# Optimization experiments

Hardware: AMD Instinct MI355X
Metric: run time of the kernel (lower is better)

Reference implementation:

```python
import jax, jax.numpy as jnp
import numpy as np

NEG = -1e30  # log-space 'zero' (avoid real -inf for stable exp/grad)


def _ctc_loss_mean(logp, targets, target_lengths, blank):
    """CTC loss, PyTorch semantics (reduction='mean', zero_infinity=True).
    logp: (B, T, V) log-probabilities; targets: (B, L) padded labels;
    target_lengths: (B,) ints. All input lengths are T (uniform here).
    """
    B, T, V = logp.shape
    L = targets.shape[1]
    S = 2 * L + 1  # extended label length: blank-interleaved

    ext = jnp.full((B, S), blank, dtype=targets.dtype)
    ext = ext.at[:, 1::2].set(targets)  # blanks at even s, labels at odd s

    s = jnp.arange(S)
    valid = s[None, :] < (2 * target_lengths + 1)[:, None]  # (B, S)
    prev2 = jnp.pad(ext[:, :-2], ((0, 0), (2, 0)), constant_values=blank)
    # skip transition s-2 -> s allowed only at non-blank s with no label repeat
    allow_skip = (s[None, :] >= 2) & (ext != blank) & (ext != prev2)

    # per-(t, s) emission log-prob, masked outside valid extended labels
    emit = jnp.take_along_axis(
        logp, jnp.broadcast_to(ext[:, None, :], (B, T, S)), axis=2
    )  # (B, T, S)
    emit = jnp.where(valid[:, None, :], emit, NEG)

    alpha0 = jnp.full((B, S), NEG, dtype=logp.dtype)
    alpha0 = alpha0.at[:, 0].set(emit[:, 0, 0])
    alpha0 = alpha0.at[:, 1].set(emit[:, 0, 1])

    def step(alpha, e):
        a1 = alpha
        a2 = jnp.pad(alpha[:, :-1], ((0, 0), (1, 0)), constant_values=NEG)
        a3 = jnp.pad(alpha[:, :-2], ((0, 0), (2, 0)), constant_values=NEG)
        a3 = jnp.where(allow_skip, a3, NEG)
        m = jnp.maximum(jnp.maximum(a1, a2), a3)
        new = m + jnp.log(jnp.exp(a1 - m) + jnp.exp(a2 - m) + jnp.exp(a3 - m)) + e
        return new, None

    alpha, _ = jax.lax.scan(step, alpha0, jnp.swapaxes(emit, 0, 1)[1:])

    i1 = (2 * target_lengths).astype(jnp.int32)
    l1 = jnp.take_along_axis(alpha, i1[:, None], axis=1)[:, 0]
    l2 = jnp.take_along_axis(alpha, jnp.maximum(i1 - 1, 0)[:, None], axis=1)[:, 0]
    l2 = jnp.where(target_lengths > 0, l2, NEG)
    m = jnp.maximum(l1, l2)
    loss = -(m + jnp.log(jnp.exp(l1 - m) + jnp.exp(l2 - m)))  # (B,)
    loss = jnp.where(loss > 1e20, 0.0, loss)  # zero_infinity=True
    # reduction='mean': divide by target length, then batch mean
    return jnp.mean(loss / jnp.maximum(target_lengths, 1).astype(loss.dtype))


def setup_inputs() -> dict:
    key = jax.random.key(0)
    kl, kt, kn = jax.random.split(key, 3)
    B, T, V, L = 32, 1024, 1000, 256
    logits = jax.random.normal(kl, (B, T, V), dtype=jnp.float32)
    targets = jax.random.randint(kt, (B, L), 1, V).astype(jnp.int32)
    lengths = jax.random.randint(kn, (B,), L // 2 + 2, L + 1)
    target_padding_mask = jnp.arange(L)[None, :] < lengths[:, None]  # bool (B, L)
    return {"logits": logits, "targets": targets,
            "target_padding_mask": target_padding_mask}


def reference(logits, targets, target_padding_mask):
    blank = 0
    lg = logits[:, :-1, :]            # drop last frame
    tgt = targets[:, 1:]              # drop leading (SOS) token
    logp = jax.nn.log_softmax(lg, axis=-1)  # (B, T-1, V)
    tlen = target_padding_mask.sum(axis=1).astype(jnp.int32) - 1
    return _ctc_loss_mean(logp, tgt, tlen, blank)
```

## Files before the change

kernel.cpp:

```cpp
#include <hip/hip_runtime.h>

#define LOG2E 1.4426950408889634f
#define LN2   0.6931471805599453

static constexpr int B  = 32;
static constexpr int T  = 1024;
static constexpr int TT = 1023;
static constexpr int V  = 1000;
static constexpr int L  = 256;
static constexpr int S  = 511;
static constexpr int SP = 512;
static constexpr int TP = 1024;

using h8  = __attribute__((ext_vector_type(8))) _Float16;
using f4  = __attribute__((ext_vector_type(4))) float;
using i4  = __attribute__((ext_vector_type(4))) int;

__device__ __forceinline__ float fexp2(float x) {
#if __has_builtin(__builtin_amdgcn_exp2f)
  return __builtin_amdgcn_exp2f(x);
#else
  return exp2f(x);
#endif
}
__device__ __forceinline__ float flog2(float x) {
#if __has_builtin(__builtin_amdgcn_logf)
  return __builtin_amdgcn_logf(x);
#else
  return log2f(x);
#endif
}

#if __has_builtin(__builtin_amdgcn_update_dpp)
__device__ __forceinline__ float shr1f(float x) {
  int r = __builtin_amdgcn_update_dpp(0, __float_as_int(x), 0x138, 0xf, 0xf, true);
  return __int_as_float(r);
}
__device__ __forceinline__ int shl1i(int x) {
  return __builtin_amdgcn_update_dpp(0, x, 0x130, 0xf, 0xf, true);
}
#define DPP_SWITCH(T, OLD, SRC, BC)                                            \
  T r;                                                                         \
  switch (ctrl) {                                                              \
    case 0x111: r = __builtin_amdgcn_update_dpp(OLD, SRC, 0x111, 0xf, 0xf, BC); break; \
    case 0x112: r = __builtin_amdgcn_update_dpp(OLD, SRC, 0x112, 0xf, 0xf, BC); break; \
    case 0x114: r = __builtin_amdgcn_update_dpp(OLD, SRC, 0x114, 0xf, 0xf, BC); break; \
    case 0x118: r = __builtin_amdgcn_update_dpp(OLD, SRC, 0x118, 0xf, 0xf, BC); break; \
    case 0x142: r = __builtin_amdgcn_update_dpp(OLD, SRC, 0x142, 0xf, 0xf, BC); break; \
    default:    r = __builtin_amdgcn_update_dpp(OLD, SRC, 0x143, 0xf, 0xf, BC); break; \
  }

__device__ __forceinline__ int dppmax_step(int m, const int ctrl) {
  DPP_SWITCH(int, 0, m, true);
  return max(m, r);
}
__device__ __forceinline__ int wavemax_to_sgpr(int m) {
  m = dppmax_step(m, 0x111);
  m = dppmax_step(m, 0x112);
  m = dppmax_step(m, 0x114);
  m = dppmax_step(m, 0x118);
  m = dppmax_step(m, 0x142);
  m = dppmax_step(m, 0x143);
  return __builtin_amdgcn_readlane(m, 63);
}
__device__ __forceinline__ float dppfmax_step(float x, const int ctrl) {
  int xi = __float_as_int(x);
  DPP_SWITCH(int, xi, xi, false);
  return fmaxf(x, __int_as_float(r));
}
__device__ __forceinline__ float wavefmax(float x) {
  x = dppfmax_step(x, 0x111);
  x = dppfmax_step(x, 0x112);
  x = dppfmax_step(x, 0x114);
  x = dppfmax_step(x, 0x118);
  x = dppfmax_step(x, 0x142);
  x = dppfmax_step(x, 0x143);
  return __int_as_float(__builtin_amdgcn_readlane(__float_as_int(x), 63));
}
__device__ __forceinline__ float dppfadd_step(float x, const int ctrl) {
  DPP_SWITCH(int, 0, __float_as_int(x), true);
  return x + __int_as_float(r);
}
__device__ __forceinline__ float wavefsum(float x) {
  x = dppfadd_step(x, 0x111);
  x = dppfadd_step(x, 0x112);
  x = dppfadd_step(x, 0x114);
  x = dppfadd_step(x, 0x118);
  x = dppfadd_step(x, 0x142);
  x = dppfadd_step(x, 0x143);
  return __int_as_float(__builtin_amdgcn_readlane(__float_as_int(x), 63));
}
#else
__device__ __forceinline__ float shr1f(float x) {
  float r = __shfl_up(x, 1, 64);
  return (threadIdx.x & 63) == 0 ? 0.0f : r;
}
__device__ __forceinline__ int shl1i(int x) {
  int r = __shfl_down(x, 1, 64);
  return (threadIdx.x & 63) == 63 ? 0 : r;
}
__device__ __forceinline__ int wavemax_to_sgpr(int m) {
  for (int o = 32; o >= 1; o >>= 1) m = max(m, __shfl_xor(m, o, 64));
  return m;
}
__device__ __forceinline__ float wavefmax(float x) {
  for (int o = 32; o >= 1; o >>= 1) x = fmaxf(x, __shfl_xor(x, o, 64));
  return x;
}
__device__ __forceinline__ float wavefsum(float x) {
  for (int o = 32; o >= 1; o >>= 1) x += __shfl_xor(x, o, 64);
  return x;
}
#endif

__global__ void k_tlen(const unsigned char* __restrict__ maskb,
                       int* __restrict__ tlen) {
  int b = blockIdx.x;
  int lane = threadIdx.x;
  int ca = 0;
  for (int k = lane; k < L; k += 64) ca += (maskb[b * L + k] != 0) ? 1 : 0;
  for (int o = 32; o >= 1; o >>= 1) ca += __shfl_xor(ca, o, 64);
  int cnt = ca;
  if (ca < 130) {
    const int* mi = (const int*)maskb;
    int cb = 0;
    for (int k = lane; k < L; k += 64) cb += (mi[b * L + k] != 0) ? 1 : 0;
    for (int o = 32; o >= 1; o >>= 1) cb += __shfl_xor(cb, o, 64);
    cnt = cb;
  }
  if (lane == 0) tlen[b] = cnt - 1;
}

__global__ __launch_bounds__(256, 4) void k_emit(const float* __restrict__ logits,
                                                 const int* __restrict__ targets,
                                                 const int* __restrict__ tlenp,
                                                 _Float16* __restrict__ E,
                                                 float* __restrict__ G) {
  __shared__ float yrow[4][1024];
  const int wid = threadIdx.x >> 6;
  const int lane = threadIdx.x & 63;
  float* yw = yrow[wid];
  const int w0 = blockIdx.x * 4 + wid;
  const int sb = lane << 3;

#define EISSUE(P, r)                                              \
  do {                                                            \
    int b_ = (r) / TT;                                            \
    int t_ = (r) - b_ * TT;                                       \
    const float* rp_ = logits + ((size_t)b_ * T + t_) * V + (lane << 2); \
    const int* tp_ = targets + b_ * L + (lane << 2);              \
    const int* lp_ = tlenp + b_;                                  \
    asm volatile(                                                 \
      "global_load_dwordx4 %0, %6, off\n\t"                       \
      "global_load_dwordx4 %1, %6, off offset:1024\n\t"           \
      "global_load_dwordx4 %2, %6, off offset:2048\n\t"           \
      "global_load_dwordx4 %3, %6, off offset:3072\n\t"           \
      "global_load_dwordx4 %4, %7, off\n\t"                       \
      "global_load_dword %5, %8, off"                             \
      : "=&v"(P##u0), "=&v"(P##u1), "=&v"(P##u2), "=&v"(P##u3),   \
        "=&v"(P##tv), "=&v"(P##tl)                                \
      : "v"(rp_), "v"(tp_), "v"(lp_));                            \
  } while (0)

#define EWAIT(n, P)                                               \
  do {                                                            \
    asm volatile("s_waitcnt vmcnt(" #n ")"                        \
                 : "+v"(P##u0), "+v"(P##u1), "+v"(P##u2),         \
                   "+v"(P##u3), "+v"(P##tv), "+v"(P##tl));        \
    __builtin_amdgcn_sched_barrier(0);                            \
  } while (0)

#define EPROC(P, r)                                               \
  do {                                                            \
    int b_ = (r) / TT;                                            \
    int t_ = (r) - b_ * TT;                                       \
    f4 v0 = P##u0 * LOG2E;                                        \
    f4 v1 = P##u1 * LOG2E;                                        \
    f4 v2 = P##u2 * LOG2E;                                        \
    f4 v3 = P##u3 * LOG2E;                                        \
    const bool has3 = (lane < 58);         \
    if (!has3) { v3[0] = v3[1] = v3[2] = v3[3] = -2.0e30f; }      \
    reinterpret_cast<f4*>(yw)[lane]       = v0;                   \
    reinterpret_cast<f4*>(yw)[lane + 64]  = v1;                   \
    reinterpret_cast<f4*>(yw)[lane + 128] = v2;                   \
    if (has3) reinterpret_cast<f4*>(yw)[lane + 192] = v3;         \
    float lm = fmaxf(fmaxf(fmaxf(v0[0], v0[1]), fmaxf(v0[2], v0[3])), \
                     fmaxf(fmaxf(v1[0], v1[1]), fmaxf(v1[2], v1[3]))); \
    lm = fmaxf(lm, fmaxf(fmaxf(v2[0], v2[1]), fmaxf(v2[2], v2[3]))); \
    lm = fmaxf(lm, fmaxf(fmaxf(v3[0], v3[1]), fmaxf(v3[2], v3[3]))); \
    const float my = wavefmax(lm);                                \
    float ps = fexp2(v0[0]-my) + fexp2(v0[1]-my) + fexp2(v0[2]-my) + fexp2(v0[3]-my) \
             + fexp2(v1[0]-my) + fexp2(v1[1]-my) + fexp2(v1[2]-my) + fexp2(v1[3]-my) \
             + fexp2(v2[0]-my) + fexp2(v2[1]-my) + fexp2(v2[2]-my) + fexp2(v2[3]-my) \
             + fexp2(v3[0]-my) + fexp2(v3[1]-my) + fexp2(v3[2]-my) + fexp2(v3[3]-my); \
    const float g = -flog2(wavefsum(ps));                         \
    const int smax = 2 * P##tl + 1;                               \
    const int l1 = P##tv[1], l2 = P##tv[2], l3 = P##tv[3];        \
    const int l4 = shl1i(P##tv[0]);              \
    const float eb = fexp2(yw[0]  - my);                          \
    const float e1 = fexp2(yw[l1] - my);                          \
    const float e2 = fexp2(yw[l2] - my);                          \
    const float e3 = fexp2(yw[l3] - my);                          \
    const float e4 = fexp2(yw[l4] - my);                          \
    h8 o;                                                         \
    o[0] = (_Float16)((sb     < smax) ? eb : 0.0f);               \
    o[1] = (_Float16)((sb + 1 < smax) ? e1 : 0.0f);               \
    o[2] = (_Float16)((sb + 2 < smax) ? eb : 0.0f);               \
    o[3] = (_Float16)((sb + 3 < smax) ? e2 : 0.0f);               \
    o[4] = (_Float16)((sb + 4 < smax) ? eb : 0.0f);               \
    o[5] = (_Float16)((sb + 5 < smax) ? e3 : 0.0f);               \
    o[6] = (_Float16)((sb + 6 < smax) ? eb : 0.0f);               \
    o[7] = (_Float16)((lane < 63 && sb + 7 < smax) ? e4 : 0.0f);  \
    reinterpret_cast<h8*>(E + ((size_t)b_ * TP + t_) * SP)[lane] = o; \
    if (lane == 0) G[r] = g;                                      \
  } while (0)

  f4 Au0, Au1, Au2, Au3; i4 Atv; int Atl;
  f4 Bu0, Bu1, Bu2, Bu3; i4 Btv; int Btl;
  f4 Cu0, Cu1, Cu2, Cu3; i4 Ctv; int Ctl;

  EISSUE(A, w0);
  EISSUE(B, w0 + 8184);
  EISSUE(C, w0 + 16368);
  EWAIT(12, A); EPROC(A, w0);
  EISSUE(A, w0 + 24552);
  EWAIT(12, B); EPROC(B, w0 + 8184);
  EWAIT(6,  C); EPROC(C, w0 + 16368);
  EWAIT(0,  A); EPROC(A, w0 + 24552);
#undef EISSUE
#undef EWAIT
#undef EPROC
}

__global__ __launch_bounds__(64, 1) void k_ctc(const _Float16* __restrict__ E,
                                               const int* __restrict__ targets,
                                               const int* __restrict__ tlenp,
                                               const float* __restrict__ G,
                                               float* __restrict__ lossb) {
  const int b = blockIdx.x;
  const int lane = threadIdx.x;
  const int s0 = lane << 3;
  const int* tg = targets + b * L;

  const int tl = tlenp[b];

  double gs = 0.0;
  for (int k = lane; k < TT; k += 64) gs += (double)G[b * TT + k];
  for (int o = 32; o >= 1; o >>= 1) gs += __shfl_xor(gs, o, 64);

  float f1 = 0.0f, f3, f5, f7 = 0.0f;
  {
    int s = s0 + 1;
    if (s >= 3) f1 = (tg[(s + 1) >> 1] != tg[(s - 1) >> 1]) ? 1.0f : 0.0f;
    s = s0 + 3;
    f3 = (tg[(s + 1) >> 1] != tg[(s - 1) >> 1]) ? 1.0f : 0.0f;
    s = s0 + 5;
    f5 = (tg[(s + 1) >> 1] != tg[(s - 1) >> 1]) ? 1.0f : 0.0f;
    s = s0 + 7;
    if (s < S) f7 = (tg[(s + 1) >> 1] != tg[(s - 1) >> 1]) ? 1.0f : 0.0f;
  }

  const _Float16* E0 = E + (size_t)b * TP * SP;
  const _Float16* Ebase = E0 + s0;

  float a0 = (lane == 0) ? (float)E0[0] : 0.0f;
  float a1 = (lane == 0) ? (float)E0[1] : 0.0f;
  float a2 = 0.f, a3 = 0.f, a4 = 0.f, a5 = 0.f, a6 = 0.f, a7 = 0.f;
  float n7 = 0.0f;
  int lsacc = 0;

  asm volatile("" :: "v"(f1), "v"(f3), "v"(f5), "v"(f7),
                     "v"(a0), "v"(a1), "v"(gs), "v"((float)tl));

#define GLROW4(d0, d1, d2, d3, p)                                \
  asm volatile("global_load_dwordx4 %0, %4, off\n\t"             \
               "global_load_dwordx4 %1, %4, off offset:1024\n\t" \
               "global_load_dwordx4 %2, %4, off offset:2048\n\t" \
               "global_load_dwordx4 %3, %4, off offset:3072"     \
               : "=&v"(d0), "=&v"(d1), "=&v"(d2), "=&v"(d3) : "v"(p))

#define LOAD8(P, r0)                                             \
  do {                                                           \
    const _Float16* q_ = Ebase + (size_t)(r0) * SP;              \
    GLROW4(P##0, P##1, P##2, P##3, q_);                          \
    GLROW4(P##4, P##5, P##6, P##7, q_ + 4 * SP);                 \
  } while (0)

#define VMWAIT8(n, P)                                            \
  do {                                                           \
    asm volatile("s_waitcnt vmcnt(" #n ")"                       \
                 : "+v"(P##0), "+v"(P##1), "+v"(P##2), "+v"(P##3), \
                   "+v"(P##4), "+v"(P##5), "+v"(P##6), "+v"(P##7)); \
    __builtin_amdgcn_sched_barrier(0);                           \
  } while (0)

#define STEPF(H)                                                \
  do {                                                          \
    float e7 = (float)(H)[7];                                   \
    float t7 = fmaf(f7, a5, a6 + a7) * e7;                      \
    float n7n = shr1f(t7);                                      \
    float e0 = (float)(H)[0], e1 = (float)(H)[1];               \
    float e2 = (float)(H)[2], e3 = (float)(H)[3];               \
    float e4 = (float)(H)[4], e5 = (float)(H)[5];               \
    float e6 = (float)(H)[6];                                   \
    float t0 = (a0 + n7) * e0;                                  \
    float t1 = fmaf(f1, n7, a0 + a1) * e1;                      \
    float t2 = (a1 + a2) * e2;                                  \
    float t3 = fmaf(f3, a1, a2 + a3) * e3;                      \
    float t4 = (a3 + a4) * e4;                                  \
    float t5 = fmaf(f5, a3, a4 + a5) * e5;                      \
    float t6 = (a5 + a6) * e6;                                  \
    a0 = t0; a1 = t1; a2 = t2; a3 = t3;                         \
    a4 = t4; a5 = t5; a6 = t6; a7 = t7;                         \
    n7 = n7n;                                                   \
  } while (0)

#define RESCALE()                                               \
  do {                                                          \
    int m = max(max(max(__float_as_int(a0), __float_as_int(a1)),\
                    max(__float_as_int(a2), __float_as_int(a3))),\
                max(max(__float_as_int(a4), __float_as_int(a5)),\
                    max(__float_as_int(a6), __float_as_int(a7))));\
    int mw = wavemax_to_sgpr(m);                                \
    int e = mw >> 23;                                           \
    int sh = 229 - e;                                           \
    lsacc += e - 229;                                           \
    a0 = ldexpf(a0, sh); a1 = ldexpf(a1, sh);                   \
    a2 = ldexpf(a2, sh); a3 = ldexpf(a3, sh);                   \
    a4 = ldexpf(a4, sh); a5 = ldexpf(a5, sh);                   \
    a6 = ldexpf(a6, sh); a7 = ldexpf(a7, sh);                   \
    n7 = ldexpf(n7, sh);                                        \
  } while (0)

#define PROC8R(P)                                               \
  do {                                                          \
    RESCALE();                                                  \
    STEPF(P##0); STEPF(P##1); STEPF(P##2); STEPF(P##3);         \
    STEPF(P##4); STEPF(P##5); STEPF(P##6); STEPF(P##7);         \
  } while (0)

  h8 A0, A1, A2, A3, A4, A5, A6, A7;
  h8 B0, B1, B2, B3, B4, B5, B6, B7;
  h8 C0, C1, C2, C3, C4, C5, C6, C7;
  h8 D0, D1, D2, D3, D4, D5, D6, D7;

  LOAD8(A, 1);
  LOAD8(B, 9);
  LOAD8(C, 17);
  LOAD8(D, 25);

  int t = 1;
#pragma unroll 1
  for (int it = 0; it < 30; ++it) {
    VMWAIT8(24, A); PROC8R(A); LOAD8(A, t + 32);
    VMWAIT8(24, B); PROC8R(B); LOAD8(B, t + 40);
    VMWAIT8(24, C); PROC8R(C); LOAD8(C, t + 48);
    VMWAIT8(24, D); PROC8R(D); LOAD8(D, t + 56);
    t += 32;
  }
  VMWAIT8(24, A); PROC8R(A); LOAD8(A, 993);
  VMWAIT8(24, B); PROC8R(B); LOAD8(B, 1001);
  VMWAIT8(24, C); PROC8R(C); LOAD8(C, 1009);
  VMWAIT8(24, D); PROC8R(D); LOAD8(D, 1017);
  VMWAIT8(24, A); PROC8R(A);
  VMWAIT8(16, B); PROC8R(B);
  VMWAIT8(8,  C); PROC8R(C);
  VMWAIT8(0,  D);
  RESCALE();
  STEPF(D0); STEPF(D1); STEPF(D2);
  STEPF(D3); STEPF(D4); STEPF(D5);
#undef GLROW4
#undef LOAD8
#undef VMWAIT8
#undef STEPF
#undef RESCALE
#undef PROC8R

  __shared__ float sal[SP];
  sal[s0 + 0] = a0; sal[s0 + 1] = a1; sal[s0 + 2] = a2; sal[s0 + 3] = a3;
  sal[s0 + 4] = a4; sal[s0 + 5] = a5; sal[s0 + 6] = a6; sal[s0 + 7] = a7;
  __syncthreads();
  if (lane == 0) {
    int i1 = 2 * tl;
    float p = sal[i1] + sal[(i1 > 0 ? i1 : 1) - 1];
    int hi = __float_as_int(p);
    int ep = (hi >> 23) - 127;
    float pm = ldexpf(p, -ep);
    float lm = flog2(pm);
    double loss2 = -((double)lm + (double)ep + (double)lsacc + gs);
    float loss = (float)(loss2 * LN2);
    if (!(loss <= 1e20f)) loss = 0.0f;
    int dv = (tl > 0) ? tl : 1;
    lossb[b] = loss / (float)dv;
  }
}

__global__ void k_mean(const float* __restrict__ lossb, float* __restrict__ out) {
  int lane = threadIdx.x;
  float v = (lane < B) ? lossb[lane] : 0.0f;
  for (int o = 32; o >= 1; o >>= 1) v += __shfl_xor(v, o, 64);
  if (lane == 0) out[0] = v / (float)B;
}

extern "C" void kernel_launch(void* const* d_in, const int* in_sizes, int n_in,
                              void* d_out, int out_size, void* d_ws, size_t ws_size,
                              hipStream_t stream) {
  const float* logits = (const float*)d_in[0];
  const int* targets = (const int*)d_in[1];
  const unsigned char* mask = (const unsigned char*)d_in[2];

  char* ws = (char*)d_ws;
  int* tlen = (int*)ws;
  float* lossb = (float*)(ws + 128);
  float* G = (float*)(ws + 512);
  _Float16* E = (_Float16*)(ws + 512 + 132 * 1024);

  k_tlen<<<B, 64, 0, stream>>>(mask, tlen);
  k_emit<<<(B * TT) / 16, 256, 0, stream>>>(logits, targets, tlen, E, G);
  k_ctc<<<B, 64, 0, stream>>>(E, targets, tlen, G, lossb);
  k_mean<<<1, 64, 0, stream>>>(lossb, (float*)d_out);
}
```

Before: 99.98 us.

## Fuse f16 emission convert into multiply via fma_mix and rescale less often

Replaces the separate f16-to-f32 convert plus multiply in each recurrence step with a single v_fma_mix_f32 that reads the packed half directly. It also moves the wave-wide max rescale from every 8 steps to every 32 steps, lowering the target exponent so the values have headroom to avoid overflow over the longer interval. The final loss gather now uses register shuffles instead of an LDS write, barrier and read. Rescaling less often risks underflow or overflow in the scaled probability domain.

```diff
diff --git a/kernel.cpp b/kernel.cpp
--- a/kernel.cpp
+++ b/kernel.cpp
@@ -294,22 +294,34 @@
     __builtin_amdgcn_sched_barrier(0);                           \
   } while (0)
 
+#define MIXLO(D, SSS, HWORD)                                     \
+  asm("v_fma_mix_f32 %0, %1, %2, 0 op_sel:[0,0,0] op_sel_hi:[0,1,0]" \
+      : "=v"(D) : "v"(SSS), "v"(HWORD))
+#define MIXHI(D, SSS, HWORD)                                     \
+  asm("v_fma_mix_f32 %0, %1, %2, 0 op_sel:[0,1,0] op_sel_hi:[0,1,0]" \
+      : "=v"(D) : "v"(SSS), "v"(HWORD))
+
 #define STEPF(H)                                                \
   do {                                                          \
-    float e7 = (float)(H)[7];                                   \
-    float t7 = fmaf(f7, a5, a6 + a7) * e7;                      \
+    i4 hw = __builtin_bit_cast(i4, (H));                        \
+    float s7 = fmaf(f7, a5, a6 + a7);                           \
+    float t7; MIXHI(t7, s7, hw[3]);                             \
     float n7n = shr1f(t7);                                      \
-    float e0 = (float)(H)[0], e1 = (float)(H)[1];               \
-    float e2 = (float)(H)[2], e3 = (float)(H)[3];               \
-    float e4 = (float)(H)[4], e5 = (float)(H)[5];               \
-    float e6 = (float)(H)[6];                                   \
-    float t0 = (a0 + n7) * e0;                                  \
-    float t1 = fmaf(f1, n7, a0 + a1) * e1;                      \
-    float t2 = (a1 + a2) * e2;                                  \
-    float t3 = fmaf(f3, a1, a2 + a3) * e3;                      \
-    float t4 = (a3 + a4) * e4;                                  \
-    float t5 = fmaf(f5, a3, a4 + a5) * e5;                      \
-    float t6 = (a5 + a6) * e6;                                  \
+    float s0 = a0 + n7;                                         \
+    float s1 = fmaf(f1, n7, a0 + a1);                           \
+    float s2 = a1 + a2;                                         \
+    float s3 = fmaf(f3, a1, a2 + a3);                           \
+    float s4 = a3 + a4;                                         \
+    float s5 = fmaf(f5, a3, a4 + a5);                           \
+    float s6 = a5 + a6;                                         \
+    float t0, t1, t2, t3, t4, t5, t6;                           \
+    MIXLO(t0, s0, hw[0]);                                       \
+    MIXHI(t1, s1, hw[0]);                                       \
+    MIXLO(t2, s2, hw[1]);                                       \
+    MIXHI(t3, s3, hw[1]);                                       \
+    MIXLO(t4, s4, hw[2]);                                       \
+    MIXHI(t5, s5, hw[2]);                                       \
+    MIXLO(t6, s6, hw[3]);                                       \
     a0 = t0; a1 = t1; a2 = t2; a3 = t3;                         \
     a4 = t4; a5 = t5; a6 = t6; a7 = t7;                         \
     n7 = n7n;                                                   \
@@ -323,8 +335,8 @@
                     max(__float_as_int(a6), __float_as_int(a7))));\
     int mw = wavemax_to_sgpr(m);                                \
     int e = mw >> 23;                                           \
-    int sh = 229 - e;                                           \
-    lsacc += e - 229;                                           \
+    int sh = 191 - e;                                           \
+    lsacc += e - 191;                                           \
     a0 = ldexpf(a0, sh); a1 = ldexpf(a1, sh);                   \
     a2 = ldexpf(a2, sh); a3 = ldexpf(a3, sh);                   \
     a4 = ldexpf(a4, sh); a5 = ldexpf(a5, sh);                   \
@@ -332,9 +344,8 @@
     n7 = ldexpf(n7, sh);                                        \
   } while (0)
 
-#define PROC8R(P)                                               \
+#define PROC8(P)                                                \
   do {                                                          \
-    RESCALE();                                                  \
     STEPF(P##0); STEPF(P##1); STEPF(P##2); STEPF(P##3);         \
     STEPF(P##4); STEPF(P##5); STEPF(P##6); STEPF(P##7);         \
   } while (0)
@@ -352,46 +363,64 @@
   int t = 1;
 #pragma unroll 1
   for (int it = 0; it < 30; ++it) {
-    VMWAIT8(24, A); PROC8R(A); LOAD8(A, t + 32);
-    VMWAIT8(24, B); PROC8R(B); LOAD8(B, t + 40);
-    VMWAIT8(24, C); PROC8R(C); LOAD8(C, t + 48);
-    VMWAIT8(24, D); PROC8R(D); LOAD8(D, t + 56);
+    RESCALE();
+    VMWAIT8(24, A); PROC8(A); LOAD8(A, t + 32);
+    VMWAIT8(24, B); PROC8(B); LOAD8(B, t + 40);
+    VMWAIT8(24, C); PROC8(C); LOAD8(C, t + 48);
+    VMWAIT8(24, D); PROC8(D); LOAD8(D, t + 56);
     t += 32;
   }
-  VMWAIT8(24, A); PROC8R(A); LOAD8(A, 993);
-  VMWAIT8(24, B); PROC8R(B); LOAD8(B, 1001);
-  VMWAIT8(24, C); PROC8R(C); LOAD8(C, 1009);
-  VMWAIT8(24, D); PROC8R(D); LOAD8(D, 1017);
-  VMWAIT8(24, A); PROC8R(A);
-  VMWAIT8(16, B); PROC8R(B);
-  VMWAIT8(8,  C); PROC8R(C);
+  RESCALE();
+  VMWAIT8(24, A); PROC8(A); LOAD8(A, 993);
+  VMWAIT8(24, B); PROC8(B); LOAD8(B, 1001);
+  VMWAIT8(24, C); PROC8(C); LOAD8(C, 1009);
+  VMWAIT8(24, D); PROC8(D); LOAD8(D, 1017);
+  RESCALE();
+  VMWAIT8(24, A); PROC8(A);
+  VMWAIT8(16, B); PROC8(B);
+  VMWAIT8(8,  C); PROC8(C);
   VMWAIT8(0,  D);
-  RESCALE();
   STEPF(D0); STEPF(D1); STEPF(D2);
   STEPF(D3); STEPF(D4); STEPF(D5);
 #undef GLROW4
 #undef LOAD8
 #undef VMWAIT8
+#undef MIXLO
+#undef MIXHI
 #undef STEPF
 #undef RESCALE
-#undef PROC8R
-
-  __shared__ float sal[SP];
-  sal[s0 + 0] = a0; sal[s0 + 1] = a1; sal[s0 + 2] = a2; sal[s0 + 3] = a3;
-  sal[s0 + 4] = a4; sal[s0 + 5] = a5; sal[s0 + 6] = a6; sal[s0 + 7] = a7;
-  __syncthreads();
-  if (lane == 0) {
+#undef PROC8
+
+  {
     int i1 = 2 * tl;
-    float p = sal[i1] + sal[(i1 > 0 ? i1 : 1) - 1];
-    int hi = __float_as_int(p);
-    int ep = (hi >> 23) - 127;
-    float pm = ldexpf(p, -ep);
-    float lm = flog2(pm);
-    double loss2 = -((double)lm + (double)ep + (double)lsacc + gs);
-    float loss = (float)(loss2 * LN2);
-    if (!(loss <= 1e20f)) loss = 0.0f;
-    int dv = (tl > 0) ? tl : 1;
-    lossb[b] = loss / (float)dv;
+    int j1 = (i1 > 0 ? i1 : 1) - 1;
+    float va, vb;
+    switch (i1 & 7) {
+      case 0: va = a0; break; case 1: va = a1; break;
+      case 2: va = a2; break; case 3: va = a3; break;
+      case 4: va = a4; break; case 5: va = a5; break;
+      case 6: va = a6; break; default: va = a7; break;
+    }
+    switch (j1 & 7) {
+      case 0: vb = a0; break; case 1: vb = a1; break;
+      case 2: vb = a2; break; case 3: vb = a3; break;
+      case 4: vb = a4; break; case 5: vb = a5; break;
+      case 6: vb = a6; break; default: vb = a7; break;
+    }
+    float l1v = __shfl(va, i1 >> 3, 64);
+    float l2v = __shfl(vb, j1 >> 3, 64);
+    if (lane == 0) {
+      float p = l1v + l2v;
+      int hi = __float_as_int(p);
+      int ep = (hi >> 23) - 127;
+      float pm = ldexpf(p, -ep);
+      float lm = flog2(pm);
+      double loss2 = -((double)lm + (double)ep + (double)lsacc + gs);
+      float loss = (float)(loss2 * LN2);
+      if (!(loss <= 1e20f)) loss = 0.0f;
+      int dv = (tl > 0) ? tl : 1;
+      lossb[b] = loss / (float)dv;
+    }
   }
 }
 
```

Result: faster. 88.32 us (-11.7%).
